# Kernel tuning notes

Hardware: AMD Instinct MI355X
Metric: run time of the kernel (lower is better)

Reference implementation:

```python
import jax, jax.numpy as jnp
import numpy as np

BN_EPS = 1e-5

def conv2d(x, w, pad):
    return jax.lax.conv_general_dilated(x, w, (1, 1), [(pad, pad), (pad, pad)],
                                        dimension_numbers=('NCHW', 'OIHW', 'NCHW'))

def bn(x, g, b, m, v):
    # eval-mode batchnorm with running stats
    c = (None, slice(None), None, None)
    return g[c] * (x - m[c]) * jax.lax.rsqrt(v[c] + BN_EPS) + b[c]

def criss_cross_attention(x, wq, wk, wv, gamma):
    # x: (B, C, H, W); q/k have reduced dim d = C//8
    B, C, H, W = x.shape
    q = jnp.einsum('bchw,dc->bdhw', x, wq)
    k = jnp.einsum('bchw,dc->bdhw', x, wk)
    v = jnp.einsum('bchw,dc->bdhw', x, wv)
    # column (vertical) affinities: for each (h,w), keys at (k,w) -> (B,H,W,H)
    eH = jnp.einsum('bdhw,bdkw->bhwk', q, k)
    # -inf on the h==k diagonal (avoid counting the center pixel twice)
    eH = eH + jnp.where(jnp.eye(H, dtype=bool), -jnp.inf, 0.0)[None, :, None, :]
    # row (horizontal) affinities: keys at (h,k) -> (B,H,W,W)
    eW = jnp.einsum('bdhw,bdhk->bhwk', q, k)
    att = jax.nn.softmax(jnp.concatenate([eH, eW], axis=3), axis=3)  # (B,H,W,H+W)
    aH, aW = att[..., :H], att[..., H:]
    oH = jnp.einsum('bhwk,bdkw->bdhw', aH, v)
    oW = jnp.einsum('bhwk,bdhk->bdhw', aW, v)
    return gamma * (oH + oW) + x

def upsample_bilinear_align_corners(x, out_h, out_w):
    # torch nn.Upsample(mode='bilinear', align_corners=True)
    def interp(x, size, axis):
        n = x.shape[axis]
        pos = jnp.arange(size, dtype=x.dtype) * ((n - 1) / (size - 1))
        lo = jnp.floor(pos).astype(jnp.int32)
        hi = jnp.minimum(lo + 1, n - 1)
        w = pos - lo.astype(x.dtype)
        shp = [1] * x.ndim; shp[axis] = size
        w = w.reshape(shp)
        return jnp.take(x, lo, axis=axis) * (1 - w) + jnp.take(x, hi, axis=axis) * w
    x = interp(x, out_h, 2)
    return interp(x, out_w, 3)

def setup_inputs() -> dict:
    key = jax.random.key(0)
    ks = jax.random.split(key, 16)
    B, C, H, W = 2, 2048, 96, 96
    ic = C // 32          # inter_c = 64
    dq = ic // 8          # 8
    nc = 19
    s = 0.05
    return {
        'x': jax.random.normal(ks[0], (B, C, H, W), jnp.float32),
        'w_in': jax.random.normal(ks[1], (ic, C, 3, 3), jnp.float32) * s,
        'bn_in_g': jnp.ones((ic,), jnp.float32),
        'bn_in_b': jnp.zeros((ic,), jnp.float32),
        'bn_in_m': jax.random.normal(ks[2], (ic,), jnp.float32) * 0.1,
        'bn_in_v': jax.random.uniform(ks[3], (ic,), jnp.float32, 0.5, 1.5),
        'wq': jax.random.normal(ks[4], (dq, ic), jnp.float32) * s,
        'wk': jax.random.normal(ks[5], (dq, ic), jnp.float32) * s,
        'wv': jax.random.normal(ks[6], (ic, ic), jnp.float32) * s,
        'cca_gamma': jax.random.uniform(ks[7], (1,), jnp.float32, 0.2, 0.8),
        'w_out': jax.random.normal(ks[8], (ic, ic, 3, 3), jnp.float32) * s,
        'bn_out_g': jnp.ones((ic,), jnp.float32),
        'bn_out_b': jnp.zeros((ic,), jnp.float32),
        'bn_out_m': jax.random.normal(ks[9], (ic,), jnp.float32) * 0.1,
        'bn_out_v': jax.random.uniform(ks[10], (ic,), jnp.float32, 0.5, 1.5),
        'w_cls1': jax.random.normal(ks[11], (ic, C + ic, 3, 3), jnp.float32) * s,
        'bn_cls_g': jnp.ones((ic,), jnp.float32),
        'bn_cls_b': jnp.zeros((ic,), jnp.float32),
        'bn_cls_m': jax.random.normal(ks[12], (ic,), jnp.float32) * 0.1,
        'bn_cls_v': jax.random.uniform(ks[13], (ic,), jnp.float32, 0.5, 1.5),
        'w_cls2': jax.random.normal(ks[14], (nc, ic, 1, 1), jnp.float32) * s,
    }

def reference(x, w_in, bn_in_g, bn_in_b, bn_in_m, bn_in_v,
              wq, wk, wv, cca_gamma,
              w_out, bn_out_g, bn_out_b, bn_out_m, bn_out_v,
              w_cls1, bn_cls_g, bn_cls_b, bn_cls_m, bn_cls_v, w_cls2):
    RECURRENCE = 2
    out = jax.nn.relu(bn(conv2d(x, w_in, 1), bn_in_g, bn_in_b, bn_in_m, bn_in_v))
    for _ in range(RECURRENCE):
        out = criss_cross_attention(out, wq, wk, wv, cca_gamma)
    out = jax.nn.relu(bn(conv2d(out, w_out, 1), bn_out_g, bn_out_b, bn_out_m, bn_out_v))
    out = jnp.concatenate([x, out], axis=1)
    # cls_seg: conv -> BN (no relu) -> upsample x8 (bilinear, align_corners) -> 1x1 conv
    out = bn(conv2d(out, w_cls1, 1), bn_cls_g, bn_cls_b, bn_cls_m, bn_cls_v)
    H, W = out.shape[2], out.shape[3]
    out = upsample_bilinear_align_corners(out, H * 8, W * 8)
    out = conv2d(out, w_cls2, 0)
    return out
```

## Files before the change

### kernel.cpp

```cpp
#include <hip/hip_runtime.h>
#include <stdint.h>

#define HW 9216

typedef float f32x4 __attribute__((ext_vector_type(4)));
typedef short s16x8 __attribute__((ext_vector_type(8)));

#define PIN() asm volatile("" ::: "memory")
#define WAITV12() asm volatile("s_waitcnt vmcnt(12)" ::: "memory")

__device__ __forceinline__ unsigned short f2bf(float f){
  union { float fv; uint32_t u; } x; x.fv = f;
  uint32_t u = x.u;
  u += 0x7fffu + ((u >> 16) & 1u);
  return (unsigned short)(u >> 16);
}
__device__ __forceinline__ float bf2f(unsigned short s){
  union { uint32_t u; float fv; } x; x.u = ((uint32_t)s) << 16;
  return x.fv;
}

__device__ __forceinline__ void gload16(const void* g, void* l){
  __builtin_amdgcn_global_load_lds(
    (const __attribute__((address_space(1))) unsigned int*)g,
    (__attribute__((address_space(3))) unsigned int*)l, 16, 0, 0);
}

__global__ __launch_bounds__(256) void transp_kernel(const float* __restrict__ x,
    unsigned short* __restrict__ xT){
  __shared__ unsigned short tl[256 * 66];
  int blk = blockIdx.x;
  int b = blk / 1152; int r = blk - b * 1152;
  int cchunk = r / 144, pxt = r - cchunk * 144;
  int c0 = cchunk * 256, px0 = pxt * 64;
  int tid = threadIdx.x;
  for (int e = tid; e < 4096; e += 256){
    int cc = e >> 4, pq = e & 15;
    float4 v4 = *(const float4*)(x + ((size_t)(b * 2048 + c0 + cc)) * HW + px0 + pq * 4);
    const float* vp = (const float*)&v4;
    #pragma unroll
    for (int j = 0; j < 4; j++) tl[cc * 66 + pq * 4 + j] = f2bf(vp[j]);
  }
  __syncthreads();
  for (int j = tid; j < 2048; j += 256){
    int px = j >> 5, oct = j & 31;
    s16x8 pk;
    #pragma unroll
    for (int t = 0; t < 8; t++) pk[t] = (short)tl[(oct * 8 + t) * 66 + px];
    *(s16x8*)(xT + ((size_t)(b * 9216 + px0 + px)) * 2048 + c0 + oct * 8) = pk;
  }
}

__global__ void packw_kernel(const float* __restrict__ w, unsigned short* __restrict__ Wp, int Cin){
  int total = 64 * Cin * 9;
  for (int i = blockIdx.x * blockDim.x + threadIdx.x; i < total; i += gridDim.x * blockDim.x){
    int c = i & 31; int r = i >> 5; int o = r & 63; int r2 = r >> 6;
    int tap = r2 % 9; int ck = r2 / 9;
    Wp[i] = f2bf(w[((size_t)o * Cin + ck * 32 + c) * 9 + tap]);
  }
}

template<int T>
__device__ __forceinline__ void tapbody(const char* hb, s16x8 (&bs)[4], f32x4 (&acc)[4][4],
    const unsigned short* wbase, int gmax, int g0, int wv, int ln, int kg){
  constexpr int dy = T / 3, dx = T - dy * 3;
  #pragma unroll
  for (int mf = 0; mf < 4; mf++){
    int p = (wv * 4 + mf + dy) * 18 + (ln + dx);
    int aoff = p * 64 + ((kg ^ (p & 3)) << 4);
    s16x8 a = *(const s16x8*)(hb + aoff);
    #pragma unroll
    for (int nf = 0; nf < 4; nf++)
      acc[mf][nf] = __builtin_amdgcn_mfma_f32_16x16x32_bf16(a, bs[nf], acc[mf][nf], 0, 0, 0);
  }
  constexpr int dck = (T + 3) / 9, dt = (T + 3) % 9;
  if (g0 + T + 3 < gmax){
    const unsigned short* wb2 = wbase + dck * 18432 + dt * 2048;
    #pragma unroll
    for (int nf = 0; nf < 4; nf++) bs[nf] = *(const s16x8*)(wb2 + nf * 512);
  }
}

__global__ __launch_bounds__(256, 2) void conv_nhwc_kernel(
    const unsigned short* __restrict__ A0, int c0stride,
    const unsigned short* __restrict__ A1, int nck0,
    const unsigned short* __restrict__ Wp,
    unsigned short* __restrict__ sl, int nchunks,
    const unsigned short* __restrict__ zp){
  int mt = blockIdx.x;
  int b = mt / 36; int r = mt - b * 36;
  int h0 = (r / 6) * 16, w0 = (r % 6) * 16;
  int KS = gridDim.y, ks = blockIdx.y;
  int c0 = (nchunks * ks) / KS, c1 = (nchunks * (ks + 1)) / KS;
  int tid = threadIdx.x, lane = tid & 63, wv = tid >> 6;
  int ln = lane & 15, kg = lane >> 4;
  __shared__ char halo[2][24576];

  int pixb0[6], pixb1[6]; bool val[6];
  #pragma unroll
  for (int rr = 0; rr < 6; rr++){
    int i = tid + rr * 256;
    int p = i >> 2, q_lds = i & 3;
    int logq = q_lds ^ (p & 3);
    int hh = p / 18, ww = p - hh * 18;
    int h = h0 - 1 + hh, w = w0 - 1 + ww;
    bool v = (i < 1296) && ((unsigned)h < 96u) && ((unsigned)w < 96u);
    val[rr] = v;
    int pix = (b * 96 + h) * 96 + w;
    pixb0[rr] = v ? (pix * c0stride * 2 + logq * 16) : 0;
    pixb1[rr] = v ? (pix * 128 + logq * 16) : 0;
  }
  const char* a0B = (const char*)A0;
  const char* a1B = (const char*)A1;
  const char* zpB = (const char*)zp;

  auto stage = [&](char* ldsB, int ck){
    bool inA0 = (ck < nck0);
    int chb0 = ck * 64, chb1 = (ck - nck0) * 64;
    #pragma unroll
    for (int rr = 0; rr < 6; rr++){
      const char* src = zpB;
      if (val[rr]) src = inA0 ? (a0B + pixb0[rr] + chb0) : (a1B + pixb1[rr] + chb1);
      gload16(src, ldsB + (tid + rr * 256) * 16);
    }
  };

  f32x4 acc[4][4];
  #pragma unroll
  for (int i = 0; i < 4; i++)
    #pragma unroll
    for (int j = 0; j < 4; j++) acc[i][j] = (f32x4)(0.f);

  s16x8 bs0[4], bs1[4], bs2[4];
  int gmax = (c1 - c0) * 9;

  stage(&halo[0][0], c0);
  PIN();
  {
    const unsigned short* w0b = Wp + (size_t)c0 * 18432 + ln * 32 + kg * 8;
    #pragma unroll
    for (int nf = 0; nf < 4; nf++){
      bs0[nf] = *(const s16x8*)(w0b + 0 * 2048 + nf * 512);
      bs1[nf] = *(const s16x8*)(w0b + 1 * 2048 + nf * 512);
      bs2[nf] = *(const s16x8*)(w0b + 2 * 2048 + nf * 512);
    }
  }
  WAITV12();
  __builtin_amdgcn_s_barrier();

  for (int ck = c0; ck < c1; ck++){
    int cur = (ck - c0) & 1;
    if (ck + 1 < c1){ stage(&halo[cur ^ 1][0], ck + 1); PIN(); }
    const unsigned short* wbase = Wp + (size_t)ck * 18432 + ln * 32 + kg * 8;
    const char* hb = &halo[cur][0];
    int g0 = (ck - c0) * 9;
    tapbody<0>(hb, bs0, acc, wbase, gmax, g0, wv, ln, kg);
    tapbody<1>(hb, bs1, acc, wbase, gmax, g0, wv, ln, kg);
    tapbody<2>(hb, bs2, acc, wbase, gmax, g0, wv, ln, kg);
    tapbody<3>(hb, bs0, acc, wbase, gmax, g0, wv, ln, kg);
    tapbody<4>(hb, bs1, acc, wbase, gmax, g0, wv, ln, kg);
    tapbody<5>(hb, bs2, acc, wbase, gmax, g0, wv, ln, kg);
    tapbody<6>(hb, bs0, acc, wbase, gmax, g0, wv, ln, kg);
    tapbody<7>(hb, bs1, acc, wbase, gmax, g0, wv, ln, kg);
    tapbody<8>(hb, bs2, acc, wbase, gmax, g0, wv, ln, kg);
    if (ck + 1 < c1){
      WAITV12();
      __builtin_amdgcn_s_barrier();
    }
  }

  unsigned short* base = sl + ((size_t)(ks * 72 + mt)) * 16384;
  #pragma unroll
  for (int mf = 0; mf < 4; mf++)
    #pragma unroll
    for (int nf = 0; nf < 4; nf++){
      int o = nf * 16 + ln;
      #pragma unroll
      for (int rr = 0; rr < 4; rr++){
        int m = wv * 64 + mf * 16 + kg * 4 + rr;
        base[m * 64 + o] = f2bf(acc[mf][nf][rr]);
      }
    }
}

__global__ __launch_bounds__(256) void bn_reduce_kernel(const unsigned short* __restrict__ sl,
    int KS, const float* __restrict__ g, const float* __restrict__ bb,
    const float* __restrict__ mm, const float* __restrict__ vv, int relu,
    unsigned short* __restrict__ out){
  int idx = blockIdx.x * 256 + threadIdx.x;
  int mt = idx >> 14, e = idx & 16383;
  int m = e >> 6, o = e & 63;
  float s = 0.f;
  for (int ks = 0; ks < KS; ks++) s += bf2f(sl[((size_t)(ks * 72 + mt)) * 16384 + e]);
  float sc = g[o] * rsqrtf(vv[o] + 1e-5f);
  float valf = (s - mm[o]) * sc + bb[o];
  if (relu) valf = fmaxf(valf, 0.f);
  int b = mt / 36; int r = mt - b * 36;
  int h = (r / 6) * 16 + (m >> 4), w = (r % 6) * 16 + (m & 15);
  out[(((size_t)b * 96 + h) * 96 + w) * 64 + o] = f2bf(valf);
}

__global__ __launch_bounds__(256) void bn_reduce_cls_kernel(const unsigned short* __restrict__ sl,
    int KS, const float* __restrict__ g, const float* __restrict__ bb,
    const float* __restrict__ mm, const float* __restrict__ vv,
    const float* __restrict__ w2, float* __restrict__ t19){
  __shared__ float yl[4][64];
  __shared__ float w2L[19 * 64];
  int tid = threadIdx.x;
  for (int i = tid; i < 1216; i += 256) w2L[i] = w2[i];
  int idx = blockIdx.x * 256 + tid;
  int mt = idx >> 14, e = idx & 16383;
  int o = e & 63;
  float s = 0.f;
  for (int ks = 0; ks < KS; ks++) s += bf2f(sl[((size_t)(ks * 72 + mt)) * 16384 + e]);
  float sc = g[o] * rsqrtf(vv[o] + 1e-5f);
  float valf = (s - mm[o]) * sc + bb[o];
  yl[tid >> 6][o] = valf;
  __syncthreads();
  if (tid < 76){
    int mq = tid / 19, j = tid - mq * 19;
    float a = 0.f;
    #pragma unroll 8
    for (int c = 0; c < 64; c++) a += w2L[j * 64 + c] * yl[mq][c];
    int m = ((blockIdx.x & 63) << 2) + mq;
    int b = mt / 36; int r = mt - b * 36;
    int h = (r / 6) * 16 + (m >> 4), w = (r % 6) * 16 + (m & 15);
    t19[((size_t)(b * 19 + j)) * HW + h * 96 + w] = a;
  }
}

__global__ __launch_bounds__(256) void cca_proj_kernel(const unsigned short* __restrict__ xin,
    const float* __restrict__ wq, const float* __restrict__ wk, const float* __restrict__ wv,
    float* __restrict__ q, float* __restrict__ k, unsigned short* __restrict__ v){
  __shared__ float wqL[512], wkL[512], wvL[4096];
  int tid = threadIdx.x;
  for (int i = tid; i < 512; i += 256){ wqL[i] = wq[i]; wkL[i] = wk[i]; }
  for (int i = tid; i < 4096; i += 256) wvL[i] = wv[i];
  __syncthreads();
  int gid = blockIdx.x * 256 + tid;
  int gp = gid >> 1, half = gid & 1;
  unsigned short xv16[64];
  #pragma unroll
  for (int t = 0; t < 8; t++)
    *(s16x8*)(&xv16[t * 8]) = *(const s16x8*)(xin + (size_t)gp * 64 + t * 8);
  float qa[4], ka[4], va[32];
  #pragma unroll
  for (int d = 0; d < 4; d++){ qa[d] = 0.f; ka[d] = 0.f; }
  #pragma unroll
  for (int d = 0; d < 32; d++) va[d] = 0.f;
  int qo = half * 4, vo = half * 32;
  #pragma unroll 4
  for (int c = 0; c < 64; c++){
    float xv = bf2f(xv16[c]);
    #pragma unroll
    for (int d = 0; d < 4; d++){ qa[d] += wqL[(qo + d) * 64 + c] * xv; ka[d] += wkL[(qo + d) * 64 + c] * xv; }
    #pragma unroll
    for (int d = 0; d < 32; d++) va[d] += wvL[(vo + d) * 64 + c] * xv;
  }
  #pragma unroll
  for (int d = 0; d < 4; d++){ q[(size_t)gp * 8 + qo + d] = qa[d]; k[(size_t)gp * 8 + qo + d] = ka[d]; }
  #pragma unroll
  for (int t = 0; t < 4; t++){
    s16x8 pk;
    #pragma unroll
    for (int j = 0; j < 8; j++) pk[j] = (short)f2bf(va[t * 8 + j]);
    *(s16x8*)(v + (size_t)gp * 64 + vo + t * 8) = pk;
  }
}

__global__ __launch_bounds__(256, 2) void cca_colE_kernel(const float* __restrict__ qT,
    const float* __restrict__ kT, float* __restrict__ ebuf){
  int blk = blockIdx.x;
  int b = blk / 192; int r = blk - b * 192; int w = r >> 1, z = r & 1;
  __shared__ float qcL[96 * 12], kcL[48 * 12];
  int tid = threadIdx.x;
  for (int i = tid; i < 768; i += 256){
    int hp = i >> 3, d = i & 7;
    qcL[hp * 12 + d] = qT[((size_t)(b * HW) + hp * 96 + w) * 8 + d];
  }
  for (int i = tid; i < 384; i += 256){
    int j = i >> 3, d = i & 7;
    kcL[j * 12 + d] = kT[((size_t)(b * HW) + (z * 48 + j) * 96 + w) * 8 + d];
  }
  __syncthreads();
  int h0 = (tid & 15) * 6, kl0 = (tid >> 4) * 3;
  f32x4 q0[6], q1[6], k0[3], k1[3];
  #pragma unroll
  for (int i = 0; i < 6; i++){
    q0[i] = *(const f32x4*)&qcL[(h0 + i) * 12];
    q1[i] = *(const f32x4*)&qcL[(h0 + i) * 12 + 4];
  }
  #pragma unroll
  for (int j = 0; j < 3; j++){
    k0[j] = *(const f32x4*)&kcL[(kl0 + j) * 12];
    k1[j] = *(const f32x4*)&kcL[(kl0 + j) * 12 + 4];
  }
  #pragma unroll
  for (int i = 0; i < 6; i++){
    size_t rbase = (((size_t)b * 96 + (h0 + i)) * 96 + w) * 96;
    #pragma unroll
    for (int j = 0; j < 3; j++){
      float e = 0.f;
      #pragma unroll
      for (int d = 0; d < 4; d++) e += q0[i][d] * k0[j][d] + q1[i][d] * k1[j][d];
      int kpg = z * 48 + kl0 + j;
      ebuf[rbase + kpg] = (kpg == h0 + i) ? -1e30f : e;
    }
  }
}

__global__ __launch_bounds__(256, 2) void cca_rowSM_kernel(const float* __restrict__ qT,
    const float* __restrict__ kT, const unsigned short* __restrict__ vT,
    const unsigned short* __restrict__ xin, const float* __restrict__ gamma,
    float* __restrict__ ebuf, unsigned short* __restrict__ xout){
  int blk = blockIdx.x;
  int b = blk / 192; int r = blk - b * 192; int h = r >> 1, z = r & 1;
  __shared__ float qrL[48 * 12], krL[96 * 12];
  __shared__ float ewT[96 * 50];
  __shared__ float vLf[96 * 68];
  __shared__ float aWf[48 * 100];
  int tid = threadIdx.x;
  int lane = tid & 63, wvid = tid >> 6;
  size_t rowb = (size_t)(b * HW) + h * 96;
  const float* ebase = ebuf + rowb * 96;

  float pre0[12], pre1[12];
  #pragma unroll
  for (int t = 0; t < 12; t++){
    int w = z * 48 + wvid + t * 4;
    pre0[t] = ebase[(size_t)w * 96 + lane];
    pre1[t] = (lane < 32) ? ebase[(size_t)w * 96 + 64 + lane] : 0.f;
  }

  for (int i = tid; i < 384; i += 256){
    int wl = i >> 3, d = i & 7;
    qrL[wl * 12 + d] = qT[(rowb + z * 48 + wl) * 8 + d];
  }
  for (int i = tid; i < 768; i += 256){
    int wp = i >> 3, d = i & 7;
    krL[wp * 12 + d] = kT[(rowb + wp) * 8 + d];
  }
  for (int i = tid; i < 768; i += 256){
    int wp = i >> 3, oct = i & 7;
    s16x8 v8 = *(const s16x8*)(vT + (rowb + wp) * 64 + oct * 8);
    #pragma unroll
    for (int j = 0; j < 8; j++) vLf[wp * 68 + oct * 8 + j] = bf2f((unsigned short)v8[j]);
  }
  __syncthreads();
  {
    int wl0 = (tid & 15) * 3, kp0 = (tid >> 4) * 6;
    f32x4 q0[3], q1[3], k0[6], k1[6];
    #pragma unroll
    for (int i = 0; i < 3; i++){
      q0[i] = *(const f32x4*)&qrL[(wl0 + i) * 12];
      q1[i] = *(const f32x4*)&qrL[(wl0 + i) * 12 + 4];
    }
    #pragma unroll
    for (int j = 0; j < 6; j++){
      k0[j] = *(const f32x4*)&krL[(kp0 + j) * 12];
      k1[j] = *(const f32x4*)&krL[(kp0 + j) * 12 + 4];
    }
    #pragma unroll
    for (int j = 0; j < 6; j++)
      #pragma unroll
      for (int i = 0; i < 3; i++){
        float e = 0.f;
        #pragma unroll
        for (int d = 0; d < 4; d++) e += q0[i][d] * k0[j][d] + q1[i][d] * k1[j][d];
        ewT[(kp0 + j) * 50 + (wl0 + i)] = e;
      }
  }
  __syncthreads();
  #pragma unroll
  for (int t = 0; t < 12; t++){
    int wl = wvid + t * 4;
    int w = z * 48 + wl;
    float x0 = pre0[t];
    float x1 = (lane < 32) ? pre1[t] : ewT[(lane - 32) * 50 + wl];
    float x2 = ewT[(lane + 32) * 50 + wl];
    float mx = fmaxf(x0, fmaxf(x1, x2));
    #pragma unroll
    for (int s = 32; s; s >>= 1) mx = fmaxf(mx, __shfl_xor(mx, s));
    float e0 = __expf(x0 - mx), e1 = __expf(x1 - mx), e2 = __expf(x2 - mx);
    float sm = e0 + e1 + e2;
    #pragma unroll
    for (int s = 32; s; s >>= 1) sm += __shfl_xor(sm, s);
    float inv = 1.f / sm;
    float* ebw = (float*)(ebase + (size_t)w * 96);
    ebw[lane] = e0 * inv;
    if (lane < 32) ebw[64 + lane] = e1 * inv;
    else           aWf[wl * 100 + (lane - 32)] = e1 * inv;
    aWf[wl * 100 + (lane + 32)] = e2 * inv;
  }
  __syncthreads();
  float gm = gamma[0];
  int d0 = (tid & 15) * 4, wl0 = (tid >> 4) * 3;
  f32x4 acc2[3];
  #pragma unroll
  for (int c = 0; c < 3; c++) acc2[c] = (f32x4)(0.f);
  for (int kp = 0; kp < 96; kp += 4){
    f32x4 a0 = *(const f32x4*)&aWf[(wl0 + 0) * 100 + kp];
    f32x4 a1 = *(const f32x4*)&aWf[(wl0 + 1) * 100 + kp];
    f32x4 a2 = *(const f32x4*)&aWf[(wl0 + 2) * 100 + kp];
    #pragma unroll
    for (int j = 0; j < 4; j++){
      f32x4 vv = *(const f32x4*)&vLf[(kp + j) * 68 + d0];
      acc2[0] += vv * a0[j];
      acc2[1] += vv * a1[j];
      acc2[2] += vv * a2[j];
    }
  }
  #pragma unroll
  for (int c = 0; c < 3; c++){
    size_t pix = rowb + z * 48 + wl0 + c;
    ushort4 xr = *(const ushort4*)&xin[pix * 64 + d0];
    ushort4 ov;
    ov.x = f2bf(bf2f(xr.x) + gm * acc2[c][0]);
    ov.y = f2bf(bf2f(xr.y) + gm * acc2[c][1]);
    ov.z = f2bf(bf2f(xr.z) + gm * acc2[c][2]);
    ov.w = f2bf(bf2f(xr.w) + gm * acc2[c][3]);
    *(ushort4*)&xout[pix * 64 + d0] = ov;
  }
}

__global__ __launch_bounds__(256, 2) void cca_colO_kernel(const unsigned short* __restrict__ vT,
    const float* __restrict__ gamma, const float* __restrict__ ebuf,
    const unsigned short* __restrict__ xpart, unsigned short* __restrict__ xout){
  int blk = blockIdx.x;
  int b = blk / 192; int r = blk - b * 192; int w = r >> 1, z = r & 1;
  __shared__ float vLf[96 * 68];
  __shared__ float aTf[48 * 100];
  int tid = threadIdx.x;
  for (int i = tid; i < 768; i += 256){
    int kp = i >> 3, oct = i & 7;
    s16x8 v8 = *(const s16x8*)(vT + ((size_t)(b * HW) + kp * 96 + w) * 64 + oct * 8);
    #pragma unroll
    for (int j = 0; j < 8; j++) vLf[kp * 68 + oct * 8 + j] = bf2f((unsigned short)v8[j]);
  }
  for (int i = tid; i < 4608; i += 256){
    int hl = i / 96, kp = i - hl * 96;
    aTf[hl * 100 + kp] = ebuf[(((size_t)b * 96 + z * 48 + hl) * 96 + w) * 96 + kp];
  }
  __syncthreads();
  float gm = gamma[0];
  int d0 = (tid & 15) * 4, hl0 = (tid >> 4) * 3;
  f32x4 acc2[3];
  #pragma unroll
  for (int c = 0; c < 3; c++) acc2[c] = (f32x4)(0.f);
  for (int kp = 0; kp < 96; kp += 4){
    f32x4 a0 = *(const f32x4*)&aTf[(hl0 + 0) * 100 + kp];
    f32x4 a1 = *(const f32x4*)&aTf[(hl0 + 1) * 100 + kp];
    f32x4 a2 = *(const f32x4*)&aTf[(hl0 + 2) * 100 + kp];
    #pragma unroll
    for (int j = 0; j < 4; j++){
      f32x4 vv = *(const f32x4*)&vLf[(kp + j) * 68 + d0];
      acc2[0] += vv * a0[j];
      acc2[1] += vv * a1[j];
      acc2[2] += vv * a2[j];
    }
  }
  #pragma unroll
  for (int c = 0; c < 3; c++){
    size_t pix = (size_t)(b * HW) + (z * 48 + hl0 + c) * 96 + w;
    ushort4 xr = *(const ushort4*)&xpart[pix * 64 + d0];
    ushort4 ov;
    ov.x = f2bf(bf2f(xr.x) + gm * acc2[c][0]);
    ov.y = f2bf(bf2f(xr.y) + gm * acc2[c][1]);
    ov.z = f2bf(bf2f(xr.z) + gm * acc2[c][2]);
    ov.w = f2bf(bf2f(xr.w) + gm * acc2[c][3]);
    *(ushort4*)&xout[pix * 64 + d0] = ov;
  }
}

__global__ void upsample_kernel(const float* __restrict__ t19, float* __restrict__ out){
  int gid = blockIdx.x * 256 + threadIdx.x;
  int xq = gid % 192; int t = gid / 192;
  int yy = t % 768; t /= 768;
  int o = t % 19; int b = t / 19;
  const float R = 95.0f / 767.0f;
  float ry = yy * R;
  int iy = (int)ry;
  float fy = ry - (float)iy;
  int iy1 = min(iy + 1, 95);
  const float* base = t19 + ((size_t)b * 19 + o) * HW;
  float4 res;
  float* rp = (float*)&res;
  #pragma unroll
  for (int j = 0; j < 4; j++){
    int xx = xq * 4 + j;
    float rx = xx * R;
    int ix = (int)rx; float fx = rx - (float)ix; int ix1 = min(ix + 1, 95);
    float v00 = base[iy * 96 + ix],  v01 = base[iy * 96 + ix1];
    float v10 = base[iy1 * 96 + ix], v11 = base[iy1 * 96 + ix1];
    rp[j] = (1.f - fy) * ((1.f - fx) * v00 + fx * v01) + fy * ((1.f - fx) * v10 + fx * v11);
  }
  *(float4*)(out + (((size_t)b * 19 + o) * 768 + yy) * 768 + xq * 4) = res;
}

extern "C" void kernel_launch(void* const* d_in, const int* in_sizes, int n_in,
                              void* d_out, int out_size, void* d_ws, size_t ws_size,
                              hipStream_t stream){
  const float* x       = (const float*)d_in[0];
  const float* w_in    = (const float*)d_in[1];
  const float* bn_in_g = (const float*)d_in[2];
  const float* bn_in_b = (const float*)d_in[3];
  const float* bn_in_m = (const float*)d_in[4];
  const float* bn_in_v = (const float*)d_in[5];
  const float* wq      = (const float*)d_in[6];
  const float* wk      = (const float*)d_in[7];
  const float* wv      = (const float*)d_in[8];
  const float* gamma   = (const float*)d_in[9];
  const float* w_out   = (const float*)d_in[10];
  const float* bn_o_g  = (const float*)d_in[11];
  const float* bn_o_b  = (const float*)d_in[12];
  const float* bn_o_m  = (const float*)d_in[13];
  const float* bn_o_v  = (const float*)d_in[14];
  const float* w_cls1  = (const float*)d_in[15];
  const float* bn_c_g  = (const float*)d_in[16];
  const float* bn_c_b  = (const float*)d_in[17];
  const float* bn_c_m  = (const float*)d_in[18];
  const float* bn_c_v  = (const float*)d_in[19];
  const float* w_cls2  = (const float*)d_in[20];
  float* out = (float*)d_out;

  char* ws = (char*)d_ws;
  size_t off = 0;
  auto alloc = [&](size_t bytes) -> void* {
    void* p = ws + off; off += (bytes + 255) & ~(size_t)255; return p;
  };
  const int KS = 12;
  const size_t NHWCb = (size_t)2 * HW * 64 * 2;
  unsigned short* xT   = (unsigned short*)alloc((size_t)2 * HW * 2048 * 2);
  unsigned short* sl   = (unsigned short*)alloc((size_t)KS * 72 * 16384 * 2);
  float* ebuf = (float*)sl;
  unsigned short* xattA = (unsigned short*)alloc(NHWCb);
  unsigned short* xattB = (unsigned short*)alloc(NHWCb);
  unsigned short* Ptmp  = (unsigned short*)alloc(NHWCb);
  unsigned short* attT  = (unsigned short*)alloc(NHWCb);
  unsigned short* midT  = (unsigned short*)alloc(NHWCb);
  float* qb    = (float*)alloc((size_t)2 * HW * 8 * 4);
  float* kb    = (float*)alloc((size_t)2 * HW * 8 * 4);
  unsigned short* vb = (unsigned short*)alloc(NHWCb);
  float* t19   = (float*)alloc((size_t)2 * 19 * HW * 4);
  unsigned short* WpIn  = (unsigned short*)alloc((size_t)64 * 2048 * 9 * 2);
  unsigned short* WpOut = (unsigned short*)alloc((size_t)64 * 64 * 9 * 2);
  unsigned short* WpCls = (unsigned short*)alloc((size_t)64 * 2112 * 9 * 2);
  unsigned short* zp    = (unsigned short*)alloc(256);
  (void)ws_size; (void)in_sizes; (void)n_in; (void)out_size;

  hipMemsetAsync(zp, 0, 256, stream);
  transp_kernel<<<2304, 256, 0, stream>>>(x, xT);
  packw_kernel<<<1024, 256, 0, stream>>>(w_in,   WpIn,  2048);
  packw_kernel<<<64,   256, 0, stream>>>(w_out,  WpOut, 64);
  packw_kernel<<<1024, 256, 0, stream>>>(w_cls1, WpCls, 2112);

  conv_nhwc_kernel<<<dim3(72, KS), 256, 0, stream>>>(xT, 2048, nullptr, 64, WpIn, sl, 64, zp);
  bn_reduce_kernel<<<4608, 256, 0, stream>>>(sl, KS, bn_in_g, bn_in_b, bn_in_m, bn_in_v, 1, xattA);

  cca_proj_kernel<<<144, 256, 0, stream>>>(xattA, wq, wk, wv, qb, kb, vb);
  cca_colE_kernel<<<384, 256, 0, stream>>>(qb, kb, ebuf);
  cca_rowSM_kernel<<<384, 256, 0, stream>>>(qb, kb, vb, xattA, gamma, ebuf, Ptmp);
  cca_colO_kernel<<<384, 256, 0, stream>>>(vb, gamma, ebuf, Ptmp, xattB);
  cca_proj_kernel<<<144, 256, 0, stream>>>(xattB, wq, wk, wv, qb, kb, vb);
  cca_colE_kernel<<<384, 256, 0, stream>>>(qb, kb, ebuf);
  cca_rowSM_kernel<<<384, 256, 0, stream>>>(qb, kb, vb, xattB, gamma, ebuf, Ptmp);
  cca_colO_kernel<<<384, 256, 0, stream>>>(vb, gamma, ebuf, Ptmp, attT);

  conv_nhwc_kernel<<<dim3(72, 2), 256, 0, stream>>>(attT, 64, nullptr, 2, WpOut, sl, 2, zp);
  bn_reduce_kernel<<<4608, 256, 0, stream>>>(sl, 2, bn_o_g, bn_o_b, bn_o_m, bn_o_v, 1, midT);

  conv_nhwc_kernel<<<dim3(72, KS), 256, 0, stream>>>(xT, 2048, midT, 64, WpCls, sl, 66, zp);
  bn_reduce_cls_kernel<<<4608, 256, 0, stream>>>(sl, KS, bn_c_g, bn_c_b, bn_c_m, bn_c_v, w_cls2, t19);

  upsample_kernel<<<21888, 256, 0, stream>>>(t19, out);
}
```

Measured before the change: 441.9 us.

## Fuse CCA q/k/v projections into preceding BN-reduce and colO kernels; merge weight packing

Removes both standalone cca_proj launches by computing q, k and v inside bn_reduce (for the first recurrence) and inside cca_colO (for the second), using the freshly computed fp32 activations held in shared memory. The three weight-packing launches are merged into one kernel. This saves launches and a re-read of the activation tensor. The cost is that every bn_reduce block (4608 of them) reloads the 4K-entry weight matrices into LDS. colO's shared memory also grows by a lot, which may reduce occupancy. The separate q2/k2/v2 buffers avoid read/write hazards.

```diff
diff --git a/kernel.cpp b/kernel.cpp
--- a/kernel.cpp
+++ b/kernel.cpp
@@ -51,12 +51,19 @@
   }
 }
 
-__global__ void packw_kernel(const float* __restrict__ w, unsigned short* __restrict__ Wp, int Cin){
-  int total = 64 * Cin * 9;
+__global__ void pack_all_kernel(const float* __restrict__ w_in, const float* __restrict__ w_out,
+    const float* __restrict__ w_cls1, unsigned short* __restrict__ WpIn,
+    unsigned short* __restrict__ WpOut, unsigned short* __restrict__ WpCls){
+  const int N0 = 64 * 2048 * 9, N1 = 64 * 64 * 9, N2 = 64 * 2112 * 9;
+  int total = N0 + N1 + N2;
   for (int i = blockIdx.x * blockDim.x + threadIdx.x; i < total; i += gridDim.x * blockDim.x){
-    int c = i & 31; int r = i >> 5; int o = r & 63; int r2 = r >> 6;
+    const float* w; unsigned short* Wp; int Cin; int idx;
+    if (i < N0){ w = w_in; Wp = WpIn; Cin = 2048; idx = i; }
+    else if (i < N0 + N1){ w = w_out; Wp = WpOut; Cin = 64; idx = i - N0; }
+    else { w = w_cls1; Wp = WpCls; Cin = 2112; idx = i - N0 - N1; }
+    int c = idx & 31; int r = idx >> 5; int o = r & 63; int r2 = r >> 6;
     int tap = r2 % 9; int ck = r2 / 9;
-    Wp[i] = f2bf(w[((size_t)o * Cin + ck * 32 + c) * 9 + tap]);
+    Wp[idx] = f2bf(w[((size_t)o * Cin + ck * 32 + c) * 9 + tap]);
   }
 }
 
@@ -186,8 +193,23 @@
 __global__ __launch_bounds__(256) void bn_reduce_kernel(const unsigned short* __restrict__ sl,
     int KS, const float* __restrict__ g, const float* __restrict__ bb,
     const float* __restrict__ mm, const float* __restrict__ vv, int relu,
-    unsigned short* __restrict__ out){
-  int idx = blockIdx.x * 256 + threadIdx.x;
+    unsigned short* __restrict__ out, int do_proj,
+    const float* __restrict__ wq, const float* __restrict__ wk, const float* __restrict__ wv,
+    float* __restrict__ q, float* __restrict__ k, unsigned short* __restrict__ v){
+  __shared__ float yl[4 * 65];
+  __shared__ float wqL[8 * 65], wkL[8 * 65], wvL[64 * 65];
+  int tid = threadIdx.x;
+  if (do_proj){
+    for (int i = tid; i < 512; i += 256){
+      int d = i >> 6, c = i & 63;
+      wqL[d * 65 + c] = wq[i]; wkL[d * 65 + c] = wk[i];
+    }
+    for (int i = tid; i < 4096; i += 256){
+      int o = i >> 6, c = i & 63;
+      wvL[o * 65 + c] = wv[i];
+    }
+  }
+  int idx = blockIdx.x * 256 + tid;
   int mt = idx >> 14, e = idx & 16383;
   int m = e >> 6, o = e & 63;
   float s = 0.f;
@@ -198,6 +220,26 @@
   int b = mt / 36; int r = mt - b * 36;
   int h = (r / 6) * 16 + (m >> 4), w = (r % 6) * 16 + (m & 15);
   out[(((size_t)b * 96 + h) * 96 + w) * 64 + o] = f2bf(valf);
+  if (do_proj){
+    int px = tid >> 6;
+    yl[px * 65 + o] = valf;
+    __syncthreads();
+    int m2 = ((blockIdx.x & 63) << 2) + px;
+    int h2 = (r / 6) * 16 + (m2 >> 4), w2 = (r % 6) * 16 + (m2 & 15);
+    size_t pix2 = ((size_t)b * 96 + h2) * 96 + w2;
+    float va = 0.f;
+    #pragma unroll 8
+    for (int c = 0; c < 64; c++) va += wvL[o * 65 + c] * yl[px * 65 + c];
+    v[pix2 * 64 + o] = f2bf(va);
+    if (o < 16){
+      const float* wsel = (o < 8) ? wqL : wkL;
+      int d = o & 7;
+      float qa = 0.f;
+      #pragma unroll 8
+      for (int c = 0; c < 64; c++) qa += wsel[d * 65 + c] * yl[px * 65 + c];
+      if (o < 8) q[pix2 * 8 + d] = qa; else k[pix2 * 8 + d] = qa;
+    }
+  }
 }
 
 __global__ __launch_bounds__(256) void bn_reduce_cls_kernel(const unsigned short* __restrict__ sl,
@@ -229,45 +271,6 @@
   }
 }
 
-__global__ __launch_bounds__(256) void cca_proj_kernel(const unsigned short* __restrict__ xin,
-    const float* __restrict__ wq, const float* __restrict__ wk, const float* __restrict__ wv,
-    float* __restrict__ q, float* __restrict__ k, unsigned short* __restrict__ v){
-  __shared__ float wqL[512], wkL[512], wvL[4096];
-  int tid = threadIdx.x;
-  for (int i = tid; i < 512; i += 256){ wqL[i] = wq[i]; wkL[i] = wk[i]; }
-  for (int i = tid; i < 4096; i += 256) wvL[i] = wv[i];
-  __syncthreads();
-  int gid = blockIdx.x * 256 + tid;
-  int gp = gid >> 1, half = gid & 1;
-  unsigned short xv16[64];
-  #pragma unroll
-  for (int t = 0; t < 8; t++)
-    *(s16x8*)(&xv16[t * 8]) = *(const s16x8*)(xin + (size_t)gp * 64 + t * 8);
-  float qa[4], ka[4], va[32];
-  #pragma unroll
-  for (int d = 0; d < 4; d++){ qa[d] = 0.f; ka[d] = 0.f; }
-  #pragma unroll
-  for (int d = 0; d < 32; d++) va[d] = 0.f;
-  int qo = half * 4, vo = half * 32;
-  #pragma unroll 4
-  for (int c = 0; c < 64; c++){
-    float xv = bf2f(xv16[c]);
-    #pragma unroll
-    for (int d = 0; d < 4; d++){ qa[d] += wqL[(qo + d) * 64 + c] * xv; ka[d] += wkL[(qo + d) * 64 + c] * xv; }
-    #pragma unroll
-    for (int d = 0; d < 32; d++) va[d] += wvL[(vo + d) * 64 + c] * xv;
-  }
-  #pragma unroll
-  for (int d = 0; d < 4; d++){ q[(size_t)gp * 8 + qo + d] = qa[d]; k[(size_t)gp * 8 + qo + d] = ka[d]; }
-  #pragma unroll
-  for (int t = 0; t < 4; t++){
-    s16x8 pk;
-    #pragma unroll
-    for (int j = 0; j < 8; j++) pk[j] = (short)f2bf(va[t * 8 + j]);
-    *(s16x8*)(v + (size_t)gp * 64 + vo + t * 8) = pk;
-  }
-}
-
 __global__ __launch_bounds__(256, 2) void cca_colE_kernel(const float* __restrict__ qT,
     const float* __restrict__ kT, float* __restrict__ ebuf){
   int blk = blockIdx.x;
@@ -425,12 +428,27 @@
 
 __global__ __launch_bounds__(256, 2) void cca_colO_kernel(const unsigned short* __restrict__ vT,
     const float* __restrict__ gamma, const float* __restrict__ ebuf,
-    const unsigned short* __restrict__ xpart, unsigned short* __restrict__ xout){
+    const unsigned short* __restrict__ xpart, unsigned short* __restrict__ xout,
+    int do_proj, const float* __restrict__ wq, const float* __restrict__ wk,
+    const float* __restrict__ wv, float* __restrict__ q2, float* __restrict__ k2,
+    unsigned short* __restrict__ v2){
   int blk = blockIdx.x;
   int b = blk / 192; int r = blk - b * 192; int w = r >> 1, z = r & 1;
   __shared__ float vLf[96 * 68];
   __shared__ float aTf[48 * 100];
+  __shared__ float xoL[48 * 65];
+  __shared__ float wqL[8 * 65], wkL[8 * 65], wvL[64 * 65];
   int tid = threadIdx.x;
+  if (do_proj){
+    for (int i = tid; i < 512; i += 256){
+      int d = i >> 6, c = i & 63;
+      wqL[d * 65 + c] = wq[i]; wkL[d * 65 + c] = wk[i];
+    }
+    for (int i = tid; i < 4096; i += 256){
+      int o = i >> 6, c = i & 63;
+      wvL[o * 65 + c] = wv[i];
+    }
+  }
   for (int i = tid; i < 768; i += 256){
     int kp = i >> 3, oct = i & 7;
     s16x8 v8 = *(const s16x8*)(vT + ((size_t)(b * HW) + kp * 96 + w) * 64 + oct * 8);
@@ -463,12 +481,45 @@
   for (int c = 0; c < 3; c++){
     size_t pix = (size_t)(b * HW) + (z * 48 + hl0 + c) * 96 + w;
     ushort4 xr = *(const ushort4*)&xpart[pix * 64 + d0];
+    float r0 = bf2f(xr.x) + gm * acc2[c][0];
+    float r1 = bf2f(xr.y) + gm * acc2[c][1];
+    float r2 = bf2f(xr.z) + gm * acc2[c][2];
+    float r3 = bf2f(xr.w) + gm * acc2[c][3];
     ushort4 ov;
-    ov.x = f2bf(bf2f(xr.x) + gm * acc2[c][0]);
-    ov.y = f2bf(bf2f(xr.y) + gm * acc2[c][1]);
-    ov.z = f2bf(bf2f(xr.z) + gm * acc2[c][2]);
-    ov.w = f2bf(bf2f(xr.w) + gm * acc2[c][3]);
+    ov.x = f2bf(r0); ov.y = f2bf(r1); ov.z = f2bf(r2); ov.w = f2bf(r3);
     *(ushort4*)&xout[pix * 64 + d0] = ov;
+    if (do_proj){
+      int hl = hl0 + c;
+      xoL[hl * 65 + d0]     = r0;
+      xoL[hl * 65 + d0 + 1] = r1;
+      xoL[hl * 65 + d0 + 2] = r2;
+      xoL[hl * 65 + d0 + 3] = r3;
+    }
+  }
+  if (do_proj){
+    __syncthreads();
+    #pragma unroll
+    for (int j = 0; j < 12; j++){
+      int idx2 = tid + j * 256;
+      int px = idx2 >> 6, o = idx2 & 63;
+      float a = 0.f;
+      #pragma unroll 8
+      for (int c = 0; c < 64; c++) a += wvL[o * 65 + c] * xoL[px * 65 + c];
+      size_t pix = (size_t)(b * HW) + (z * 48 + px) * 96 + w;
+      v2[pix * 64 + o] = f2bf(a);
+    }
+    #pragma unroll
+    for (int j = 0; j < 3; j++){
+      int idx3 = tid + j * 256;
+      int px = idx3 >> 4, dd = idx3 & 15;
+      const float* wsel = (dd < 8) ? wqL : wkL;
+      int d = dd & 7;
+      float a = 0.f;
+      #pragma unroll 8
+      for (int c = 0; c < 64; c++) a += wsel[d * 65 + c] * xoL[px * 65 + c];
+      size_t pix = (size_t)(b * HW) + (z * 48 + px) * 96 + w;
+      if (dd < 8) q2[pix * 8 + d] = a; else k2[pix * 8 + d] = a;
+    }
   }
 }
 
@@ -541,6 +592,9 @@
   float* qb    = (float*)alloc((size_t)2 * HW * 8 * 4);
   float* kb    = (float*)alloc((size_t)2 * HW * 8 * 4);
   unsigned short* vb = (unsigned short*)alloc(NHWCb);
+  float* qb2   = (float*)alloc((size_t)2 * HW * 8 * 4);
+  float* kb2   = (float*)alloc((size_t)2 * HW * 8 * 4);
+  unsigned short* vb2 = (unsigned short*)alloc(NHWCb);
   float* t19   = (float*)alloc((size_t)2 * 19 * HW * 4);
   unsigned short* WpIn  = (unsigned short*)alloc((size_t)64 * 2048 * 9 * 2);
   unsigned short* WpOut = (unsigned short*)alloc((size_t)64 * 64 * 9 * 2);
@@ -550,24 +604,24 @@
 
   hipMemsetAsync(zp, 0, 256, stream);
   transp_kernel<<<2304, 256, 0, stream>>>(x, xT);
-  packw_kernel<<<1024, 256, 0, stream>>>(w_in,   WpIn,  2048);
-  packw_kernel<<<64,   256, 0, stream>>>(w_out,  WpOut, 64);
-  packw_kernel<<<1024, 256, 0, stream>>>(w_cls1, WpCls, 2112);
+  pack_all_kernel<<<2048, 256, 0, stream>>>(w_in, w_out, w_cls1, WpIn, WpOut, WpCls);
 
   conv_nhwc_kernel<<<dim3(72, KS), 256, 0, stream>>>(xT, 2048, nullptr, 64, WpIn, sl, 64, zp);
-  bn_reduce_kernel<<<4608, 256, 0, stream>>>(sl, KS, bn_in_g, bn_in_b, bn_in_m, bn_in_v, 1, xattA);
-
-  cca_proj_kernel<<<144, 256, 0, stream>>>(xattA, wq, wk, wv, qb, kb, vb);
+  bn_reduce_kernel<<<4608, 256, 0, stream>>>(sl, KS, bn_in_g, bn_in_b, bn_in_m, bn_in_v, 1,
+      xattA, 1, wq, wk, wv, qb, kb, vb);
+
   cca_colE_kernel<<<384, 256, 0, stream>>>(qb, kb, ebuf);
   cca_rowSM_kernel<<<384, 256, 0, stream>>>(qb, kb, vb, xattA, gamma, ebuf, Ptmp);
-  cca_colO_kernel<<<384, 256, 0, stream>>>(vb, gamma, ebuf, Ptmp, xattB);
-  cca_proj_kernel<<<144, 256, 0, stream>>>(xattB, wq, wk, wv, qb, kb, vb);
-  cca_colE_kernel<<<384, 256, 0, stream>>>(qb, kb, ebuf);
-  cca_rowSM_kernel<<<384, 256, 0, stream>>>(qb, kb, vb, xattB, gamma, ebuf, Ptmp);
-  cca_colO_kernel<<<384, 256, 0, stream>>>(vb, gamma, ebuf, Ptmp, attT);
+  cca_colO_kernel<<<384, 256, 0, stream>>>(vb, gamma, ebuf, Ptmp, xattB,
+      1, wq, wk, wv, qb2, kb2, vb2);
+  cca_colE_kernel<<<384, 256, 0, stream>>>(qb2, kb2, ebuf);
+  cca_rowSM_kernel<<<384, 256, 0, stream>>>(qb2, kb2, vb2, xattB, gamma, ebuf, Ptmp);
+  cca_colO_kernel<<<384, 256, 0, stream>>>(vb2, gamma, ebuf, Ptmp, attT,
+      0, wq, wk, wv, qb2, kb2, vb2);
 
   conv_nhwc_kernel<<<dim3(72, 2), 256, 0, stream>>>(attT, 64, nullptr, 2, WpOut, sl, 2, zp);
-  bn_reduce_kernel<<<4608, 256, 0, stream>>>(sl, 2, bn_o_g, bn_o_b, bn_o_m, bn_o_v, 1, midT);
+  bn_reduce_kernel<<<4608, 256, 0, stream>>>(sl, 2, bn_o_g, bn_o_b, bn_o_m, bn_o_v, 1,
+      midT, 0, wq, wk, wv, qb, kb, vb);
 
   conv_nhwc_kernel<<<dim3(72, KS), 256, 0, stream>>>(xT, 2048, midT, 64, WpCls, sl, 66, zp);
   bn_reduce_cls_kernel<<<4608, 256, 0, stream>>>(sl, KS, bn_c_g, bn_c_b, bn_c_m, bn_c_v, w_cls2, t19);
```

After: 546.9 us. 23.8% more time.
